# Kernel optimization log

Hardware: AMD Instinct MI355X
Metric: run time of the kernel (lower is better)

Reference implementation:

```python
import jax, jax.numpy as jnp
import numpy as np

H = 128
W = 128
DELTA = 7000.0  # sigmainv in the original (delta default 7000)


def setup_inputs() -> dict:
    key = jax.random.key(0)
    k1, k2, k3, k4 = jax.random.split(key, 4)
    B, P, F, TH, TW = 2, 300, 512, 512, 512
    points_bxpx3 = jax.random.uniform(k1, (B, P, 3), jnp.float32) * 2.0 - 1.0  # NDC cube [-1,1]
    faces_fx3 = jax.random.randint(k2, (F, 3), 0, P, dtype=jnp.int32)
    uv_bxpx2 = jax.random.uniform(k3, (B, P, 2), jnp.float32)  # texcoords in [0,1]
    texture_bx3xthxtw = jax.random.uniform(k4, (B, 3, TH, TW), jnp.float32)
    return {"points_bxpx3": points_bxpx3, "faces_fx3": faces_fx3,
            "uv_bxpx2": uv_bxpx2, "texture_bx3xthxtw": texture_bx3xthxtw}


def _edge(ax, ay, bx, by, px, py):
    # signed area * 2 of triangle (a, b, p); standard edge function
    return (bx - ax) * (py - ay) - (by - ay) * (px - ax)


def _seg_d2(ax, ay, bx, by, px, py):
    # squared distance from point p to segment (a, b)
    abx, aby = bx - ax, by - ay
    apx, apy = px - ax, py - ay
    denom = abx * abx + aby * aby + 1e-12
    t = jnp.clip((apx * abx + apy * aby) / denom, 0.0, 1.0)
    dx = apx - t * abx
    dy = apy - t * aby
    return dx * dx + dy * dy


def _rasterize(points_bxpx3, faces_fx3, feats_bxfx3xd, height, width, delta):
    """Soft DIB-R-style rasterizer.
    Returns (imfeat [B,H,W,D], improb [B,H,W,1]).
    """
    B = points_bxpx3.shape[0]
    v = points_bxpx3[:, faces_fx3]                      # (B,F,3,3) gathered face vertices
    x0, x1, x2 = (v[:, :, i, 0][:, :, None, None] for i in range(3))
    y0, y1, y2 = (v[:, :, i, 1][:, :, None, None] for i in range(3))
    z0, z1, z2 = (v[:, :, i, 2][:, :, None, None] for i in range(3))

    # pixel-center grid in NDC; y flipped (top row = +1)
    px = ((jnp.arange(width, dtype=points_bxpx3.dtype) + 0.5) / width * 2.0 - 1.0)[None, None, None, :]
    py = (1.0 - (jnp.arange(height, dtype=points_bxpx3.dtype) + 0.5) / height * 2.0)[None, None, :, None]

    area = _edge(x0, y0, x1, y1, x2, y2)                # (B,F,1,1) == normal_z (cross-product z)
    front = area > 1e-8                                  # front-facing (normalz > 0) cull
    inv_area = 1.0 / jnp.where(front, area, 1.0)

    w0 = _edge(x1, y1, x2, y2, px, py) * inv_area        # (B,F,H,W) barycentrics
    w1 = _edge(x2, y2, x0, y0, px, py) * inv_area
    w2 = _edge(x0, y0, x1, y1, px, py) * inv_area
    inside = front & (w0 >= 0) & (w1 >= 0) & (w2 >= 0)

    z_pix = w0 * z0 + w1 * z1 + w2 * z2                  # interpolated depth
    zbuf = jnp.where(inside, z_pix, -1e9)
    best = jnp.argmax(zbuf, axis=1)                      # (B,H,W) nearest covering face
    hit = jnp.any(inside, axis=1)[..., None].astype(points_bxpx3.dtype)  # (B,H,W,1)

    # gather winning barycentrics and per-face vertex features
    w = jnp.stack([w0, w1, w2], axis=-1)                 # (B,F,H,W,3)
    idx = jnp.broadcast_to(best[:, None, :, :, None], (B, 1, height, width, 3))
    wb = jnp.take_along_axis(w, idx, axis=1)[:, 0]       # (B,H,W,3)
    fb = jax.vmap(lambda f, i: f[i])(feats_bxfx3xd, best)  # (B,H,W,3,D)
    imfeat = jnp.einsum('bhwk,bhwkd->bhwd', wb, fb) * hit

    # soft coverage: prob of each face = exp(-delta * d2(pixel, triangle)); z-buffer blend
    d2 = jnp.minimum(
        jnp.minimum(_seg_d2(x0, y0, x1, y1, px, py), _seg_d2(x1, y1, x2, y2, px, py)),
        _seg_d2(x2, y2, x0, y0, px, py))
    d2 = jnp.where(inside, 0.0, d2)
    p = jnp.where(front, jnp.exp(-delta * d2), 0.0)      # (B,F,H,W)
    log_miss = jnp.sum(jnp.log1p(-jnp.clip(p, 0.0, 1.0 - 1e-7)), axis=1)  # (B,H,W)
    improb = (1.0 - jnp.exp(log_miss))[..., None]
    return imfeat, improb


def _fragmentshader(imtexcoords, texture_bx3xthxtw, hardmask):
    # bilinear texture sampling; background is zero
    B, C, TH, TW = texture_bx3xthxtw.shape
    u = jnp.clip(imtexcoords[..., 0], 0.0, 1.0)
    vv = jnp.clip(imtexcoords[..., 1], 0.0, 1.0)
    fx = u * (TW - 1)
    fy = (1.0 - vv) * (TH - 1)
    x0 = jnp.floor(fx).astype(jnp.int32); x1 = jnp.minimum(x0 + 1, TW - 1)
    y0 = jnp.floor(fy).astype(jnp.int32); y1 = jnp.minimum(y0 + 1, TH - 1)
    wx = (fx - x0)[:, None]; wy = (fy - y0)[:, None]     # (B,1,H,W)

    def g(tex, yy, xx):  # tex (C,TH,TW), yy/xx (H,W) -> (C,H,W)
        return tex[:, yy, xx]
    c00 = jax.vmap(g)(texture_bx3xthxtw, y0, x0)
    c01 = jax.vmap(g)(texture_bx3xthxtw, y0, x1)
    c10 = jax.vmap(g)(texture_bx3xthxtw, y1, x0)
    c11 = jax.vmap(g)(texture_bx3xthxtw, y1, x1)
    col = (c00 * (1 - wx) * (1 - wy) + c01 * wx * (1 - wy)
           + c10 * (1 - wx) * wy + c11 * wx * wy)        # (B,C,H,W)
    return col.transpose(0, 2, 3, 1) * hardmask          # (B,H,W,C)


def reference(points_bxpx3, faces_fx3, uv_bxpx2, texture_bx3xthxtw):
    # texture mode: per-face vertex features = [u, v, mask=1]
    uvf = uv_bxpx2[:, faces_fx3]                          # (B,F,3,2)
    ones = jnp.ones_like(uvf[..., :1])
    feats = jnp.concatenate([uvf, ones], axis=-1)         # (B,F,3,3)
    imfeat, improb = _rasterize(points_bxpx3, faces_fx3, feats, H, W, DELTA)
    imtexcoords = imfeat[..., :2]
    hardmask = jax.lax.stop_gradient(imfeat[..., 2:3])    # .detach() in the original
    imrender = _fragmentshader(imtexcoords, texture_bx3xthxtw, hardmask)
    return imrender, improb
```

## Files before the change

### kernel.cpp

```cpp
#include <hip/hip_runtime.h>
#include <math.h>

constexpr int kB = 2, kP = 300, kF = 512, kH = 128, kW = 128, kTH = 512, kTW = 512;
constexpr float kDelta = 7000.0f;
constexpr float kCut = 0.06f;
constexpr float kLogInside = -15.9423847f;

__device__ __forceinline__ float seg_d2(float apx, float apy, float abx, float aby) {
    float len2 = fmaf(abx, abx, aby * aby) + 1e-12f;
    float t = fmaf(apx, abx, apy * aby) * __builtin_amdgcn_rcpf(len2);
    t = fminf(fmaxf(t, 0.0f), 1.0f);
    float dx = fmaf(-t, abx, apx);
    float dy = fmaf(-t, aby, apy);
    return fmaf(dx, dx, dy * dy);
}

__global__ __launch_bounds__(512) void render_all(const float* __restrict__ pts,
                                                  const int* __restrict__ faces,
                                                  const float* __restrict__ uvs,
                                                  const float* __restrict__ tex,
                                                  float* __restrict__ out) {
    __shared__ float4 s_hot4[kF * 4];
    __shared__ float4 s_vtx4[kF * 2];
    __shared__ unsigned s_bb[kF];
    __shared__ int s_wsum[8];
    __shared__ float s_bz[512];
    __shared__ int s_bi[512];
    __shared__ float s_lm[512];

    int tile = (int)blockIdx.x;
    int b = tile >> 8;
    int rem = tile & 255;
    int ty = rem >> 4, tx = rem & 15;
    int tid = (int)threadIdx.x;
    int lane = tid & 63;
    int wv = tid >> 6;

    {
        int f = tid;
        int i0 = faces[f * 3 + 0], i1 = faces[f * 3 + 1], i2 = faces[f * 3 + 2];
        const float* pb = pts + b * kP * 3;
        float x0 = pb[i0 * 3], y0 = pb[i0 * 3 + 1], z0 = pb[i0 * 3 + 2];
        float x1 = pb[i1 * 3], y1 = pb[i1 * 3 + 1], z1 = pb[i1 * 3 + 2];
        float x2 = pb[i2 * 3], y2 = pb[i2 * 3 + 1], z2 = pb[i2 * 3 + 2];
        float area = (x1 - x0) * (y2 - y0) - (y1 - y0) * (x2 - x0);
        bool front = area > 1e-8f;

        s_bb[f] = 1u;
        unsigned long long bal = __ballot(front);
        if (lane == 0) s_wsum[wv] = __popcll(bal);
        __syncthreads();

        int base = 0;
#pragma unroll
        for (int w = 0; w < 8; ++w) base += (w < wv) ? s_wsum[w] : 0;
        int slot = base + __popcll(bal & ((1ull << lane) - 1ull));

        if (front) {
            float inv_a = 1.0f / area;
            float e0x = x2 - x1, e0y = y2 - y1;
            float e1x = x0 - x2, e1y = y0 - y2;
            float e2x = x1 - x0, e2y = y1 - y0;
            float a0 = -e0y * inv_a, b0 = e0x * inv_a, c0 = (e0y * x1 - e0x * y1) * inv_a;
            float a1 = -e1y * inv_a, b1 = e1x * inv_a, c1 = (e1y * x2 - e1x * y2) * inv_a;
            float a2 = -e2y * inv_a, b2 = e2x * inv_a, c2 = (e2y * x0 - e2x * y0) * inv_a;
            float l0 = fmaf(e0x, e0x, e0y * e0y);
            float l1 = fmaf(e1x, e1x, e1y * e1y);
            float l2 = fmaf(e2x, e2x, e2y * e2y);
            s_hot4[slot * 4 + 0] = make_float4(a0, b0, c0, a1);
            s_hot4[slot * 4 + 1] = make_float4(b1, c1, a2, b2);
            s_hot4[slot * 4 + 2] = make_float4(c2,
                                               a0 * z0 + a1 * z1 + a2 * z2,
                                               b0 * z0 + b1 * z1 + b2 * z2,
                                               c0 * z0 + c1 * z1 + c2 * z2);
            s_hot4[slot * 4 + 3] = make_float4(area * rsqrtf(l0 + 1e-12f),
                                               area * rsqrtf(l1 + 1e-12f),
                                               area * rsqrtf(l2 + 1e-12f),
                                               __int_as_float(f));
            s_vtx4[slot * 2 + 0] = make_float4(x0, y0, x1, y1);
            s_vtx4[slot * 2 + 1] = make_float4(x2, y2, 0.0f, 0.0f);
            float bx0 = fminf(fminf(x0, x1), x2) - kCut;
            float bx1 = fmaxf(fmaxf(x0, x1), x2) + kCut;
            float by0 = fminf(fminf(y0, y1), y2) - kCut;
            float by1 = fmaxf(fmaxf(y0, y1), y2) + kCut;
            int txl = (int)ceilf((64.0f * (bx0 + 1.0f) - 7.5f) * 0.125f - 1e-4f);
            int txh = (int)floorf((64.0f * (bx1 + 1.0f) - 0.5f) * 0.125f + 1e-4f);
            int tyl = (int)ceilf((64.0f * (1.0f - by1) - 7.5f) * 0.125f - 1e-4f);
            int tyh = (int)floorf((64.0f * (1.0f - by0) - 0.5f) * 0.125f + 1e-4f);
            txl = max(txl, 0); tyl = max(tyl, 0);
            txh = min(txh, 15); tyh = min(tyh, 15);
            unsigned pk = (txl > txh || tyl > tyh)
                              ? 1u
                              : ((unsigned)txl | ((unsigned)txh << 4) |
                                 ((unsigned)tyl << 8) | ((unsigned)tyh << 12));
            s_bb[slot] = pk;
        }
    }
    __syncthreads();

    int pyi = ty * 8 + (lane >> 3);
    int pxi = tx * 8 + (lane & 7);
    float px = ((float)pxi + 0.5f) * (2.0f / 128.0f) - 1.0f;
    float py = 1.0f - ((float)pyi + 0.5f) * (2.0f / 128.0f);

    unsigned bbv = s_bb[(lane << 3) + wv];
    bool ov = ((int)(bbv & 15u) <= tx) & (tx <= (int)((bbv >> 4) & 15u)) &
              ((int)((bbv >> 8) & 15u) <= ty) & (ty <= (int)((bbv >> 12) & 15u));
    unsigned long long m = __ballot(ov);

    float bestz = -1e9f;
    int besti = -1, icnt = 0;
    float lm = 0.0f;

    while (m) {
        int l = (int)__builtin_ctzll(m);
        m &= (m - 1);
        int fs = (l << 3) + wv;
        float4 h0 = s_hot4[fs * 4 + 0];
        float4 h1 = s_hot4[fs * 4 + 1];
        float4 h2 = s_hot4[fs * 4 + 2];
        float4 h3 = s_hot4[fs * 4 + 3];
        float w0 = fmaf(h0.x, px, fmaf(h0.y, py, h0.z));
        float w1 = fmaf(h0.w, px, fmaf(h1.x, py, h1.y));
        float w2 = fmaf(h1.z, px, fmaf(h1.w, py, h2.x));
        float minw = fminf(fminf(w0, w1), w2);
        bool inside = minw >= 0.0f;
        float z = fmaf(h2.y, px, fmaf(h2.z, py, h2.w));
        if (inside && z > bestz) { bestz = z; besti = fs; }
        icnt += inside ? 1 : 0;
        float db = fminf(fminf(fabsf(w0) * h3.x, fabsf(w1) * h3.y), fabsf(w2) * h3.z);
        bool need = (!inside) & (db < kCut);
        if (__any(need)) {
            float4 v01 = s_vtx4[fs * 2 + 0];
            float4 v2_ = s_vtx4[fs * 2 + 1];
            float e2x = v01.z - v01.x, e2y = v01.w - v01.y;
            float e0x = v2_.x - v01.z, e0y = v2_.y - v01.w;
            float e1x = v01.x - v2_.x, e1y = v01.y - v2_.y;
            float dA = seg_d2(px - v01.x, py - v01.y, e2x, e2y);
            float dB = seg_d2(px - v01.z, py - v01.w, e0x, e0y);
            float dC = seg_d2(px - v2_.x, py - v2_.y, e1x, e1y);
            float d2 = fminf(fminf(dA, dB), dC);
            float p = __expf(-kDelta * d2);
            p = fminf(p, 1.0f - 1e-7f);
            float lp = __logf(1.0f - p);
            lm += need ? lp : 0.0f;
        }
    }
    lm = fmaf((float)icnt, kLogInside, lm);

    s_bz[tid] = bestz;
    s_bi[tid] = besti;
    s_lm[tid] = lm;
    __syncthreads();

    if (tid < 64) {
        float bz = s_bz[tid];
        int bi = s_bi[tid];
        float L = s_lm[tid];
#pragma unroll
        for (int w = 1; w < 8; ++w) {
            float z2 = s_bz[w * 64 + tid];
            int ii = s_bi[w * 64 + tid];
            L += s_lm[w * 64 + tid];
            if (z2 > bz || (z2 == bz && ii >= 0 && (unsigned)ii < (unsigned)bi)) {
                bz = z2; bi = ii;
            }
        }
        float improb = 1.0f - expf(L);
        float u = 0.0f, v = 0.0f, mk = 0.0f;
        if (bi >= 0) {
            float4 h0 = s_hot4[bi * 4 + 0];
            float4 h1 = s_hot4[bi * 4 + 1];
            float4 h3 = s_hot4[bi * 4 + 3];
            float c2v = s_hot4[bi * 4 + 2].x;
            float w0 = fmaf(h0.x, px, fmaf(h0.y, py, h0.z));
            float w1 = fmaf(h0.w, px, fmaf(h1.x, py, h1.y));
            float w2 = fmaf(h1.z, px, fmaf(h1.w, py, c2v));
            int of = __float_as_int(h3.w);
            int j0 = faces[of * 3], j1 = faces[of * 3 + 1], j2 = faces[of * 3 + 2];
            const float* ub = uvs + b * kP * 2;
            u = w0 * ub[j0 * 2] + w1 * ub[j1 * 2] + w2 * ub[j2 * 2];
            v = w0 * ub[j0 * 2 + 1] + w1 * ub[j1 * 2 + 1] + w2 * ub[j2 * 2 + 1];
            mk = w0 + w1 + w2;
        }
        float uc = fminf(fmaxf(u, 0.0f), 1.0f);
        float vc = fminf(fmaxf(v, 0.0f), 1.0f);
        float fx = uc * (float)(kTW - 1);
        float fy = (1.0f - vc) * (float)(kTH - 1);
        int xi0 = (int)floorf(fx), yi0 = (int)floorf(fy);
        int xi1 = min(xi0 + 1, kTW - 1), yi1 = min(yi0 + 1, kTH - 1);
        float wx = fx - (float)xi0, wy = fy - (float)yi0;
        float w00 = (1.0f - wx) * (1.0f - wy);
        float w01 = wx * (1.0f - wy);
        float w10 = (1.0f - wx) * wy;
        float w11 = wx * wy;
        int o00 = yi0 * kTW + xi0, o01 = yi0 * kTW + xi1;
        int o10 = yi1 * kTW + xi0, o11 = yi1 * kTW + xi1;
        const float* tb = tex + (size_t)b * 3 * kTH * kTW;
        float cols[3];
#pragma unroll
        for (int c = 0; c < 3; ++c) {
            const float* tc = tb + c * kTH * kTW;
            cols[c] = (tc[o00] * w00 + tc[o01] * w01 + tc[o10] * w10 + tc[o11] * w11) * mk;
        }
        int pix = (b * kH + pyi) * kW + pxi;
        out[pix * 3 + 0] = cols[0];
        out[pix * 3 + 1] = cols[1];
        out[pix * 3 + 2] = cols[2];
        out[kB * kH * kW * 3 + pix] = improb;
    }
}

extern "C" void kernel_launch(void* const* d_in, const int* in_sizes, int n_in,
                              void* d_out, int out_size, void* d_ws, size_t ws_size,
                              hipStream_t stream) {
    const float* pts = (const float*)d_in[0];
    const int* faces = (const int*)d_in[1];
    const float* uvs = (const float*)d_in[2];
    const float* tex = (const float*)d_in[3];
    float* out = (float*)d_out;
    render_all<<<kB * 256, 512, 0, stream>>>(pts, faces, uvs, tex, out);
}
```

Measured before the change: 18.53 us.

## Store distance-normalized edge functions and cull faces by tile-center edge distance

Edge-function coefficients are pre-scaled by each edge's inverse length, so the per-pixel values are signed distances. This drops the separate height multipliers and lets the inside test and the cutoff test share them. Tile culling no longer uses packed bounding boxes; each face's edge distances are evaluated at the tile center against a fixed threshold. Faces are now split contiguously across waves, and the per-face record shrinks from 4 to 3 float4s with the vertex cache removed. The soft-edge distance reuses the squared edge distance when the pixel projects onto the segment, otherwise the nearest-vertex distance, and vertices are reloaded from global memory when needed. This cuts LDS use and ALU work, but adds global gathers in the soft path and the final shading, and the threshold cull may be looser or numerically fragile.

```diff
diff --git a/kernel.cpp b/kernel.cpp
--- a/kernel.cpp
+++ b/kernel.cpp
@@ -4,25 +4,16 @@
 constexpr int kB = 2, kP = 300, kF = 512, kH = 128, kW = 128, kTH = 512, kTW = 512;
 constexpr float kDelta = 7000.0f;
 constexpr float kCut = 0.06f;
+constexpr float kThr = 0.1374f;
 constexpr float kLogInside = -15.9423847f;
 
-__device__ __forceinline__ float seg_d2(float apx, float apy, float abx, float aby) {
-    float len2 = fmaf(abx, abx, aby * aby) + 1e-12f;
-    float t = fmaf(apx, abx, apy * aby) * __builtin_amdgcn_rcpf(len2);
-    t = fminf(fmaxf(t, 0.0f), 1.0f);
-    float dx = fmaf(-t, abx, apx);
-    float dy = fmaf(-t, aby, apy);
-    return fmaf(dx, dx, dy * dy);
-}
-
-__global__ __launch_bounds__(512) void render_all(const float* __restrict__ pts,
-                                                  const int* __restrict__ faces,
-                                                  const float* __restrict__ uvs,
-                                                  const float* __restrict__ tex,
-                                                  float* __restrict__ out) {
-    __shared__ float4 s_hot4[kF * 4];
-    __shared__ float4 s_vtx4[kF * 2];
-    __shared__ unsigned s_bb[kF];
+__global__ __launch_bounds__(512, 8) void render_all(const float* __restrict__ pts,
+                                                     const int* __restrict__ faces,
+                                                     const float* __restrict__ uvs,
+                                                     const float* __restrict__ tex,
+                                                     float* __restrict__ out) {
+    __shared__ float4 s_hot4[kF * 3];
+    __shared__ unsigned short s_of[kF];
     __shared__ int s_wsum[8];
     __shared__ float s_bz[512];
     __shared__ int s_bi[512];
@@ -46,7 +37,7 @@
         float area = (x1 - x0) * (y2 - y0) - (y1 - y0) * (x2 - x0);
         bool front = area > 1e-8f;
 
-        s_bb[f] = 1u;
+        s_hot4[f * 3 + 0] = make_float4(0.0f, 0.0f, -1e30f, 0.0f);
         unsigned long long bal = __ballot(front);
         if (lane == 0) s_wsum[wv] = __popcll(bal);
         __syncthreads();
@@ -61,39 +52,26 @@
             float e0x = x2 - x1, e0y = y2 - y1;
             float e1x = x0 - x2, e1y = y0 - y2;
             float e2x = x1 - x0, e2y = y1 - y0;
+            float l0 = fmaf(e0x, e0x, e0y * e0y);
+            float l1 = fmaf(e1x, e1x, e1y * e1y);
+            float l2 = fmaf(e2x, e2x, e2y * e2y);
+            float h0s = area * rsqrtf(l0 + 1e-12f);
+            float h1s = area * rsqrtf(l1 + 1e-12f);
+            float h2s = area * rsqrtf(l2 + 1e-12f);
+            float s0 = inv_a * h0s, s1 = inv_a * h1s, s2 = inv_a * h2s;
+            float A0 = -e0y * s0, B0 = e0x * s0, C0 = (e0y * x1 - e0x * y1) * s0;
+            float A1 = -e1y * s1, B1 = e1x * s1, C1 = (e1y * x2 - e1x * y2) * s1;
+            float A2 = -e2y * s2, B2 = e2x * s2, C2 = (e2y * x0 - e2x * y0) * s2;
             float a0 = -e0y * inv_a, b0 = e0x * inv_a, c0 = (e0y * x1 - e0x * y1) * inv_a;
             float a1 = -e1y * inv_a, b1 = e1x * inv_a, c1 = (e1y * x2 - e1x * y2) * inv_a;
             float a2 = -e2y * inv_a, b2 = e2x * inv_a, c2 = (e2y * x0 - e2x * y0) * inv_a;
-            float l0 = fmaf(e0x, e0x, e0y * e0y);
-            float l1 = fmaf(e1x, e1x, e1y * e1y);
-            float l2 = fmaf(e2x, e2x, e2y * e2y);
-            s_hot4[slot * 4 + 0] = make_float4(a0, b0, c0, a1);
-            s_hot4[slot * 4 + 1] = make_float4(b1, c1, a2, b2);
-            s_hot4[slot * 4 + 2] = make_float4(c2,
+            s_hot4[slot * 3 + 0] = make_float4(A0, B0, C0, A1);
+            s_hot4[slot * 3 + 1] = make_float4(B1, C1, A2, B2);
+            s_hot4[slot * 3 + 2] = make_float4(C2,
                                                a0 * z0 + a1 * z1 + a2 * z2,
                                                b0 * z0 + b1 * z1 + b2 * z2,
                                                c0 * z0 + c1 * z1 + c2 * z2);
-            s_hot4[slot * 4 + 3] = make_float4(area * rsqrtf(l0 + 1e-12f),
-                                               area * rsqrtf(l1 + 1e-12f),
-                                               area * rsqrtf(l2 + 1e-12f),
-                                               __int_as_float(f));
-            s_vtx4[slot * 2 + 0] = make_float4(x0, y0, x1, y1);
-            s_vtx4[slot * 2 + 1] = make_float4(x2, y2, 0.0f, 0.0f);
-            float bx0 = fminf(fminf(x0, x1), x2) - kCut;
-            float bx1 = fmaxf(fmaxf(x0, x1), x2) + kCut;
-            float by0 = fminf(fminf(y0, y1), y2) - kCut;
-            float by1 = fmaxf(fmaxf(y0, y1), y2) + kCut;
-            int txl = (int)ceilf((64.0f * (bx0 + 1.0f) - 7.5f) * 0.125f - 1e-4f);
-            int txh = (int)floorf((64.0f * (bx1 + 1.0f) - 0.5f) * 0.125f + 1e-4f);
-            int tyl = (int)ceilf((64.0f * (1.0f - by1) - 7.5f) * 0.125f - 1e-4f);
-            int tyh = (int)floorf((64.0f * (1.0f - by0) - 0.5f) * 0.125f + 1e-4f);
-            txl = max(txl, 0); tyl = max(tyl, 0);
-            txh = min(txh, 15); tyh = min(tyh, 15);
-            unsigned pk = (txl > txh || tyl > tyh)
-                              ? 1u
-                              : ((unsigned)txl | ((unsigned)txh << 4) |
-                                 ((unsigned)tyl << 8) | ((unsigned)tyh << 12));
-            s_bb[slot] = pk;
+            s_of[slot] = (unsigned short)f;
         }
     }
     __syncthreads();
@@ -103,43 +81,64 @@
     float px = ((float)pxi + 0.5f) * (2.0f / 128.0f) - 1.0f;
     float py = 1.0f - ((float)pyi + 0.5f) * (2.0f / 128.0f);
 
-    unsigned bbv = s_bb[(lane << 3) + wv];
-    bool ov = ((int)(bbv & 15u) <= tx) & (tx <= (int)((bbv >> 4) & 15u)) &
-              ((int)((bbv >> 8) & 15u) <= ty) & (ty <= (int)((bbv >> 12) & 15u));
-    unsigned long long m = __ballot(ov);
+    {
+    }
+    float cx = (float)(tx * 8 + 4) * (2.0f / 128.0f) - 1.0f;
+    float cy = 1.0f - (float)(ty * 8 + 4) * (2.0f / 128.0f);
+    int slt = (wv << 6) + lane;
+    float4 g0 = s_hot4[slt * 3 + 0];
+    float4 g1 = s_hot4[slt * 3 + 1];
+    float4 g2 = s_hot4[slt * 3 + 2];
+    float Lc0 = fmaf(g0.x, cx, fmaf(g0.y, cy, g0.z));
+    float Lc1 = fmaf(g0.w, cx, fmaf(g1.x, cy, g1.y));
+    float Lc2 = fmaf(g1.z, cx, fmaf(g1.w, cy, g2.x));
+    float minc = fminf(fminf(Lc0, Lc1), Lc2);
+    unsigned long long m = __ballot(minc >= -kThr);
 
     float bestz = -1e9f;
     int besti = -1, icnt = 0;
     float lm = 0.0f;
+    const float* pb = pts + b * kP * 3;
 
     while (m) {
         int l = (int)__builtin_ctzll(m);
         m &= (m - 1);
-        int fs = (l << 3) + wv;
-        float4 h0 = s_hot4[fs * 4 + 0];
-        float4 h1 = s_hot4[fs * 4 + 1];
-        float4 h2 = s_hot4[fs * 4 + 2];
-        float4 h3 = s_hot4[fs * 4 + 3];
-        float w0 = fmaf(h0.x, px, fmaf(h0.y, py, h0.z));
-        float w1 = fmaf(h0.w, px, fmaf(h1.x, py, h1.y));
-        float w2 = fmaf(h1.z, px, fmaf(h1.w, py, h2.x));
-        float minw = fminf(fminf(w0, w1), w2);
-        bool inside = minw >= 0.0f;
+        int fs = (wv << 6) + l;
+        float4 h0 = s_hot4[fs * 3 + 0];
+        float4 h1 = s_hot4[fs * 3 + 1];
+        float4 h2 = s_hot4[fs * 3 + 2];
+        float L0 = fmaf(h0.x, px, fmaf(h0.y, py, h0.z));
+        float L1 = fmaf(h0.w, px, fmaf(h1.x, py, h1.y));
+        float L2 = fmaf(h1.z, px, fmaf(h1.w, py, h2.x));
+        float minL = fminf(fminf(L0, L1), L2);
+        bool inside = minL >= 0.0f;
         float z = fmaf(h2.y, px, fmaf(h2.z, py, h2.w));
         if (inside && z > bestz) { bestz = z; besti = fs; }
         icnt += inside ? 1 : 0;
-        float db = fminf(fminf(fabsf(w0) * h3.x, fabsf(w1) * h3.y), fabsf(w2) * h3.z);
+        float db = fminf(fminf(fabsf(L0), fabsf(L1)), fabsf(L2));
         bool need = (!inside) & (db < kCut);
         if (__any(need)) {
-            float4 v01 = s_vtx4[fs * 2 + 0];
-            float4 v2_ = s_vtx4[fs * 2 + 1];
-            float e2x = v01.z - v01.x, e2y = v01.w - v01.y;
-            float e0x = v2_.x - v01.z, e0y = v2_.y - v01.w;
-            float e1x = v01.x - v2_.x, e1y = v01.y - v2_.y;
-            float dA = seg_d2(px - v01.x, py - v01.y, e2x, e2y);
-            float dB = seg_d2(px - v01.z, py - v01.w, e0x, e0y);
-            float dC = seg_d2(px - v2_.x, py - v2_.y, e1x, e1y);
-            float d2 = fminf(fminf(dA, dB), dC);
+            int of = __builtin_amdgcn_readfirstlane((int)s_of[fs]);
+            int j0 = faces[of * 3], j1 = faces[of * 3 + 1], j2 = faces[of * 3 + 2];
+            float x0 = pb[j0 * 3], y0 = pb[j0 * 3 + 1];
+            float x1 = pb[j1 * 3], y1 = pb[j1 * 3 + 1];
+            float x2 = pb[j2 * 3], y2 = pb[j2 * 3 + 1];
+            float e0x = x2 - x1, e0y = y2 - y1;
+            float e1x = x0 - x2, e1y = y0 - y2;
+            float e2x = x1 - x0, e2y = y1 - y0;
+            float p0x = px - x0, p0y = py - y0;
+            float p1x = px - x1, p1y = py - y1;
+            float p2x = px - x2, p2y = py - y2;
+            float dot0 = fmaf(p1x, e0x, p1y * e0y), len0 = fmaf(e0x, e0x, e0y * e0y);
+            float dot1 = fmaf(p2x, e1x, p2y * e1y), len1 = fmaf(e1x, e1x, e1y * e1y);
+            float dot2 = fmaf(p0x, e2x, p0y * e2y), len2 = fmaf(e2x, e2x, e2y * e2y);
+            float c0 = (dot0 >= 0.0f && dot0 <= len0) ? L0 * L0 : 1e30f;
+            float c1 = (dot1 >= 0.0f && dot1 <= len1) ? L1 * L1 : 1e30f;
+            float c2 = (dot2 >= 0.0f && dot2 <= len2) ? L2 * L2 : 1e30f;
+            float dv0 = fmaf(p0x, p0x, p0y * p0y);
+            float dv1 = fmaf(p1x, p1x, p1y * p1y);
+            float dv2 = fmaf(p2x, p2x, p2y * p2y);
+            float d2 = fminf(fminf(fminf(c0, c1), fminf(c2, dv0)), fminf(dv1, dv2));
             float p = __expf(-kDelta * d2);
             p = fminf(p, 1.0f - 1e-7f);
             float lp = __logf(1.0f - p);
@@ -169,15 +168,16 @@
         float improb = 1.0f - expf(L);
         float u = 0.0f, v = 0.0f, mk = 0.0f;
         if (bi >= 0) {
-            float4 h0 = s_hot4[bi * 4 + 0];
-            float4 h1 = s_hot4[bi * 4 + 1];
-            float4 h3 = s_hot4[bi * 4 + 3];
-            float c2v = s_hot4[bi * 4 + 2].x;
-            float w0 = fmaf(h0.x, px, fmaf(h0.y, py, h0.z));
-            float w1 = fmaf(h0.w, px, fmaf(h1.x, py, h1.y));
-            float w2 = fmaf(h1.z, px, fmaf(h1.w, py, c2v));
-            int of = __float_as_int(h3.w);
+            int of = (int)s_of[bi];
             int j0 = faces[of * 3], j1 = faces[of * 3 + 1], j2 = faces[of * 3 + 2];
+            float x0 = pb[j0 * 3], y0 = pb[j0 * 3 + 1];
+            float x1 = pb[j1 * 3], y1 = pb[j1 * 3 + 1];
+            float x2 = pb[j2 * 3], y2 = pb[j2 * 3 + 1];
+            float area = (x1 - x0) * (y2 - y0) - (y1 - y0) * (x2 - x0);
+            float inv_a = 1.0f / area;
+            float w0 = ((x2 - x1) * (py - y1) - (y2 - y1) * (px - x1)) * inv_a;
+            float w1 = ((x0 - x2) * (py - y2) - (y0 - y2) * (px - x2)) * inv_a;
+            float w2 = ((x1 - x0) * (py - y0) - (y1 - y0) * (px - x0)) * inv_a;
             const float* ub = uvs + b * kP * 2;
             u = w0 * ub[j0 * 2] + w1 * ub[j1 * 2] + w2 * ub[j2 * 2];
             v = w0 * ub[j0 * 2 + 1] + w1 * ub[j1 * 2 + 1] + w2 * ub[j2 * 2 + 1];
```

Result: slower. 22.73 us (+22.7%).
